# Performance work log

Hardware: AMD Instinct MI355X
Metric: run time of the kernel (lower is better)

Reference implementation:

```python
import jax, jax.numpy as jnp
import numpy as np

B, L, D = 2, 2048, 1024
H, DK, DV = 16, 64, 64
EPS = 1e-6


def setup_inputs() -> dict:
    key = jax.random.key(0)
    ks = jax.random.split(key, 7)
    s = 0.02
    return {
        "x": jax.random.normal(ks[0], (B, L, D), dtype=jnp.float32),
        "Wq": jax.random.normal(ks[1], (D, H * DK), dtype=jnp.float32) * s,
        "Wk": jax.random.normal(ks[2], (D, H * DK), dtype=jnp.float32) * s,
        "Wv": jax.random.normal(ks[3], (D, H * DV), dtype=jnp.float32) * s,
        "Wo": jax.random.normal(ks[4], (H * DV, D), dtype=jnp.float32) * s,
        "ln_gamma": jnp.ones((D,), dtype=jnp.float32),
        "ln_beta": jnp.zeros((D,), dtype=jnp.float32),
    }


def reference(x, Wq, Wk, Wv, Wo, ln_gamma, ln_beta):
    temp = jnp.asarray(DK, x.dtype) ** 0.5
    # projections -> [B, H, L, Dh]
    q = (x @ Wq).reshape(B, L, H, DK).transpose(0, 2, 1, 3)
    k = (x @ Wk).reshape(B, L, H, DK).transpose(0, 2, 1, 3)
    v = (x @ Wv).reshape(B, L, H, DV).transpose(0, 2, 1, 3)
    # naive attention: explicit [B,H,L,L] scores (dropout rate 0 -> identity)
    scores = jnp.einsum("bhqd,bhkd->bhqk", q / temp, k)
    attn = jax.nn.softmax(scores, axis=-1)
    o = jnp.einsum("bhqk,bhkd->bhqd", attn, v)
    o = o.transpose(0, 2, 1, 3).reshape(B, L, H * DV)
    out = o @ Wo + x  # residual
    # LayerNorm(eps=1e-6)
    mu = jnp.mean(out, axis=-1, keepdims=True)
    var = jnp.var(out, axis=-1, keepdims=True)
    return (out - mu) * jax.lax.rsqrt(var + EPS) * ln_gamma + ln_beta
```

## Files before the change

kernel.cpp:

```cpp
#include <hip/hip_runtime.h>


typedef __bf16 bf16;
typedef __bf16 bf16x2 __attribute__((ext_vector_type(2)));
typedef __bf16 bf16x4 __attribute__((ext_vector_type(4)));
typedef __bf16 bf16x8 __attribute__((ext_vector_type(8)));
typedef float floatx4 __attribute__((ext_vector_type(4)));
typedef int intx4 __attribute__((ext_vector_type(4)));

#define MFMA16(a, b, c) __builtin_amdgcn_mfma_f32_16x16x32_bf16((a), (b), (c), 0, 0, 0)

__device__ __forceinline__ void gll16(const bf16* g, bf16* l) {
  __builtin_amdgcn_global_load_lds((const __attribute__((address_space(1))) void*)g,
                                   (__attribute__((address_space(3))) void*)l, 16, 0, 0);
}

__global__ __launch_bounds__(256) void k_prep_x(const float* __restrict__ x, bf16* __restrict__ xb) {
  const int i = (blockIdx.x * 256 + threadIdx.x) * 4;
  const float4 v = *reinterpret_cast<const float4*>(x + i);
  bf16x4 o = {(bf16)v.x, (bf16)v.y, (bf16)v.z, (bf16)v.w};
  *reinterpret_cast<bf16x4*>(xb + i) = o;
}

__global__ __launch_bounds__(256) void k_prep_w(const float* __restrict__ Wq, const float* __restrict__ Wk,
                                                const float* __restrict__ Wv, const float* __restrict__ Wo,
                                                bf16* __restrict__ WT) {
  __shared__ float tile[32][33];
  const int z = blockIdx.z;
  const float* W = (z == 0) ? Wq : (z == 1) ? Wk : (z == 2) ? Wv : Wo;
  const int n0 = blockIdx.x * 32, k0 = blockIdx.y * 32;
  const int tx = threadIdx.x, ty = threadIdx.y;
#pragma unroll
  for (int j = 0; j < 32; j += 8)
    tile[ty + j][tx] = W[(size_t)(k0 + ty + j) * 1024 + n0 + tx];
  __syncthreads();
#pragma unroll
  for (int j = 0; j < 32; j += 8)
    WT[(size_t)(z * 1024 + n0 + ty + j) * 1024 + k0 + tx] = (bf16)tile[tx][ty + j];
}

template <int MODE>
__global__ __launch_bounds__(256) void k_gemm(const bf16* __restrict__ A, const bf16* __restrict__ Bt,
                                              const float* __restrict__ X, float* __restrict__ Y,
                                              bf16* __restrict__ QB, bf16* __restrict__ KB,
                                              bf16* __restrict__ VTB) {
  __shared__ __align__(16) bf16 As[128 * 64];
  __shared__ __align__(16) bf16 Bs[128 * 64];
  const int t = threadIdx.x;
  const int lane = t & 63, wv = t >> 6;
  const int qd = lane >> 4, col = lane & 15;
  const int c7 = col & 7;
  const int wm = wv >> 1, wn = wv & 1;
  const int m0 = blockIdx.x * 128, n0 = blockIdx.y * 128;
  const int srow = wv * 8 + (lane >> 3);
  const int scol = ((lane & 7) ^ (lane >> 3)) * 8;
  const bf16* Ag = A + (size_t)(m0 + srow) * 1024 + scol;
  const bf16* Bg = Bt + (size_t)(n0 + srow) * 1024 + scol;

  floatx4 acc[4][4] = {};

  for (int kt = 0; kt < 1024; kt += 64) {
    __syncthreads();
#pragma unroll
    for (int rd = 0; rd < 4; rd++) {
      gll16(Ag + (size_t)rd * 32 * 1024 + kt, As + (rd * 32 + wv * 8) * 64);
      gll16(Bg + (size_t)rd * 32 * 1024 + kt, Bs + (rd * 32 + wv * 8) * 64);
    }
    __syncthreads();
#pragma unroll
    for (int ks = 0; ks < 2; ks++) {
      bf16x8 af[4], bfr[4];
#pragma unroll
      for (int i = 0; i < 4; i++)
        af[i] = *reinterpret_cast<const bf16x8*>(As + (wm * 64 + i * 16 + col) * 64 + ((ks * 4 + qd) ^ c7) * 8);
#pragma unroll
      for (int i = 0; i < 4; i++)
        bfr[i] = *reinterpret_cast<const bf16x8*>(Bs + (wn * 64 + i * 16 + col) * 64 + ((ks * 4 + qd) ^ c7) * 8);
#pragma unroll
      for (int i = 0; i < 4; i++)
#pragma unroll
        for (int j = 0; j < 4; j++)
          acc[i][j] = MFMA16(af[i], bfr[j], acc[i][j]);
    }
  }

#pragma unroll
  for (int i = 0; i < 4; i++) {
#pragma unroll
    for (int j = 0; j < 4; j++) {
      const int mb = m0 + wm * 64 + i * 16 + qd * 4;
      const int n = n0 + wn * 64 + j * 16 + col;
      if (MODE == 0) {
        const int seg = n >> 10;
        const int h = (n & 1023) >> 6, dd = n & 63;
#pragma unroll
        for (int r = 0; r < 4; r++) {
          const int m = mb + r;
          const int bb = m >> 11, l = m & 2047;
          const float v = acc[i][j][r];
          if (seg == 0)
            QB[((size_t)(bb * 16 + h) * 2048 + l) * 64 + dd] = (bf16)(v * 0.18033688f);
          else if (seg == 1)
            KB[((size_t)(bb * 16 + h) * 2048 + l) * 64 + dd] = (bf16)v;
          else
            VTB[((size_t)(bb * 16 + h) * 64 + dd) * 2048 + l] = (bf16)v;
        }
      } else {
#pragma unroll
        for (int r = 0; r < 4; r++) {
          const int m = mb + r;
          Y[(size_t)m * 1024 + n] = acc[i][j][r] + X[(size_t)m * 1024 + n];
        }
      }
    }
  }
}

__global__ __launch_bounds__(256) void k_attn(const bf16* __restrict__ QB, const bf16* __restrict__ KB,
                                              const bf16* __restrict__ VTB, bf16* __restrict__ OB) {
  __shared__ __align__(16) bf16 Ks0[64 * 64];
  __shared__ __align__(16) bf16 Vs0[64 * 64];
  __shared__ __align__(16) bf16 Ks1[64 * 64];
  __shared__ __align__(16) bf16 Vs1[64 * 64];
  const int t = threadIdx.x;
  const int lane = t & 63, wv = t >> 6;
  const int qd = lane >> 4, col = lane & 15;
  const int c7 = col & 7;
  const int bh = blockIdx.y;
  const int qr = blockIdx.x * 128 + wv * 32;
  const int lrow0 = wv * 8 + (lane >> 3);
  const int swz = ((lane & 7) ^ (lane >> 3)) * 8;
  const int kg0 = ((lrow0 >> 5) << 5) + (((lrow0 >> 2) & 3) << 3) + (((lrow0 >> 4) & 1) << 2) + (lrow0 & 3);
  const int r1 = lrow0 + 32;
  const int kg1 = ((r1 >> 5) << 5) + (((r1 >> 2) & 3) << 3) + (((r1 >> 4) & 1) << 2) + (r1 & 3);
  const bf16* Kg0 = KB + ((size_t)bh * 2048 + kg0) * 64 + swz;
  const bf16* Kg1 = KB + ((size_t)bh * 2048 + kg1) * 64 + swz;
  const bf16* Vg0 = VTB + ((size_t)bh * 64 + lrow0) * 2048 + swz;
  const bf16* Vg1 = VTB + ((size_t)bh * 64 + lrow0 + 32) * 2048 + swz;

  bf16x8 bQ[2][2];
#pragma unroll
  for (int qt = 0; qt < 2; qt++)
#pragma unroll
    for (int s = 0; s < 2; s++)
      bQ[qt][s] = *reinterpret_cast<const bf16x8*>(QB + ((size_t)bh * 2048 + qr + qt * 16 + col) * 64 + s * 32 + qd * 8);

  floatx4 oacc[2][4] = {};
  float lsum[2] = {0.f, 0.f};
  floatx4 scur[2][4];
  int pk[2][4][2];

#define STAGE_TO(KD, VD, i)                               \
  do {                                                    \
    gll16(Kg0 + (size_t)(i) * 4096, KD + (wv * 8) * 64);  \
    gll16(Kg1 + (size_t)(i) * 4096, KD + (32 + wv * 8) * 64); \
    gll16(Vg0 + (i) * 64, VD + (wv * 8) * 64);            \
    gll16(Vg1 + (i) * 64, VD + (32 + wv * 8) * 64);       \
  } while (0)

#define QK_FROM(ks_)                                                                                  \
  do {                                                                                                \
    _Pragma("unroll") for (int nt = 0; nt < 4; nt++) {                                                \
      bf16x8 a0 = *reinterpret_cast<const bf16x8*>(ks_ + (nt * 16 + col) * 64 + (qd ^ c7) * 8);       \
      bf16x8 a1 = *reinterpret_cast<const bf16x8*>(ks_ + (nt * 16 + col) * 64 + ((4 + qd) ^ c7) * 8); \
      _Pragma("unroll") for (int qt = 0; qt < 2; qt++) {                                              \
        floatx4 z = {0.f, 0.f, 0.f, 0.f};                                                             \
        z = MFMA16(a0, bQ[qt][0], z);                                                                 \
        z = MFMA16(a1, bQ[qt][1], z);                                                                 \
        scur[qt][nt] = z;                                                                             \
      }                                                                                               \
    }                                                                                                 \
  } while (0)

#define EXPPACK()                                                                               \
  do {                                                                                          \
    _Pragma("unroll") for (int qt = 0; qt < 2; qt++) {                                          \
      _Pragma("unroll") for (int nt = 0; nt < 4; nt++) {                                        \
        const float e0 = exp2f(scur[qt][nt][0]), e1 = exp2f(scur[qt][nt][1]);                   \
        const float e2 = exp2f(scur[qt][nt][2]), e3 = exp2f(scur[qt][nt][3]);                   \
        lsum[qt] += (e0 + e1) + (e2 + e3);                                                      \
        bf16x2 p01, p23;                                                                        \
        p01[0] = (bf16)e0; p01[1] = (bf16)e1;                                                   \
        p23[0] = (bf16)e2; p23[1] = (bf16)e3;                                                   \
        pk[qt][nt][0] = __builtin_bit_cast(int, p01);                                           \
        pk[qt][nt][1] = __builtin_bit_cast(int, p23);                                           \
      }                                                                                         \
    }                                                                                           \
  } while (0)

#define PV_FROM(vs_)                                                                                  \
  do {                                                                                                \
    bf16x8 bV[4][2];                                                                                  \
    _Pragma("unroll") for (int nd = 0; nd < 4; nd++) {                                                \
      bV[nd][0] = *reinterpret_cast<const bf16x8*>(vs_ + (nd * 16 + col) * 64 + (qd ^ c7) * 8);       \
      bV[nd][1] = *reinterpret_cast<const bf16x8*>(vs_ + (nd * 16 + col) * 64 + ((4 + qd) ^ c7) * 8); \
    }                                                                                                 \
    _Pragma("unroll") for (int qt = 0; qt < 2; qt++) {                                                \
      _Pragma("unroll") for (int s = 0; s < 2; s++) {                                                 \
        intx4 w;                                                                                      \
        w[0] = pk[qt][2 * s][0]; w[1] = pk[qt][2 * s][1];                                             \
        w[2] = pk[qt][2 * s + 1][0]; w[3] = pk[qt][2 * s + 1][1];                                     \
        const bf16x8 aP = __builtin_bit_cast(bf16x8, w);                                              \
        _Pragma("unroll") for (int nd = 0; nd < 4; nd++)                                              \
          oacc[qt][nd] = MFMA16(aP, bV[nd][s], oacc[qt][nd]);                                         \
      }                                                                                               \
    }                                                                                                 \
  } while (0)

  STAGE_TO(Ks0, Vs0, 0);
  __syncthreads();
  for (int ii = 0; ii < 16; ii++) {
    const int i1 = 2 * ii + 1;
    STAGE_TO(Ks1, Vs1, i1);
    QK_FROM(Ks0);
    EXPPACK();
    PV_FROM(Vs0);
    __syncthreads();
    if (i1 < 31) STAGE_TO(Ks0, Vs0, i1 + 1);
    QK_FROM(Ks1);
    EXPPACK();
    PV_FROM(Vs1);
    __syncthreads();
  }

#pragma unroll
  for (int qt = 0; qt < 2; qt++) {
    lsum[qt] += __shfl_xor(lsum[qt], 16);
    lsum[qt] += __shfl_xor(lsum[qt], 32);
  }
  const int bb = bh >> 4, h = bh & 15;
#pragma unroll
  for (int qt = 0; qt < 2; qt++) {
#pragma unroll
    for (int r = 0; r < 4; r++) {
      const float linv = 1.f / __shfl(lsum[qt], qd * 4 + r);
      const size_t m = (size_t)bb * 2048 + qr + qt * 16 + qd * 4 + r;
#pragma unroll
      for (int nd = 0; nd < 4; nd++)
        OB[m * 1024 + h * 64 + nd * 16 + col] = (bf16)(oacc[qt][nd][r] * linv);
    }
  }
#undef STAGE_TO
#undef QK_FROM
#undef EXPPACK
#undef PV_FROM
}

__global__ __launch_bounds__(256) void k_ln(const float* __restrict__ Yin, const float* __restrict__ gamma,
                                            const float* __restrict__ beta, float* __restrict__ out) {
  __shared__ float red[8];
  const int row = blockIdx.x, t = threadIdx.x;
  const float4 v = *reinterpret_cast<const float4*>(Yin + (size_t)row * 1024 + t * 4);
  float s = v.x + v.y + v.z + v.w;
  float ss = v.x * v.x + v.y * v.y + v.z * v.z + v.w * v.w;
#pragma unroll
  for (int d = 1; d < 64; d <<= 1) {
    s += __shfl_xor(s, d);
    ss += __shfl_xor(ss, d);
  }
  if ((t & 63) == 0) {
    red[t >> 6] = s;
    red[4 + (t >> 6)] = ss;
  }
  __syncthreads();
  s = red[0] + red[1] + red[2] + red[3];
  ss = red[4] + red[5] + red[6] + red[7];
  const float mu = s * (1.f / 1024.f);
  const float var = ss * (1.f / 1024.f) - mu * mu;
  const float rs = rsqrtf(var + 1e-6f);
  const float4 g = *reinterpret_cast<const float4*>(gamma + t * 4);
  const float4 bt = *reinterpret_cast<const float4*>(beta + t * 4);
  float4 o;
  o.x = (v.x - mu) * rs * g.x + bt.x;
  o.y = (v.y - mu) * rs * g.y + bt.y;
  o.z = (v.z - mu) * rs * g.z + bt.z;
  o.w = (v.w - mu) * rs * g.w + bt.w;
  *reinterpret_cast<float4*>(out + (size_t)row * 1024 + t * 4) = o;
}

extern "C" void kernel_launch(void* const* d_in, const int* in_sizes, int n_in,
                              void* d_out, int out_size, void* d_ws, size_t ws_size,
                              hipStream_t stream) {
  (void)in_sizes; (void)n_in; (void)out_size; (void)ws_size;
  const float* x = (const float*)d_in[0];
  const float* Wq = (const float*)d_in[1];
  const float* Wk = (const float*)d_in[2];
  const float* Wv = (const float*)d_in[3];
  const float* Wo = (const float*)d_in[4];
  const float* gamma = (const float*)d_in[5];
  const float* beta = (const float*)d_in[6];

  char* ws = (char*)d_ws;
  const size_t MB = 1ull << 20;
  bf16* XB = (bf16*)(ws);
  bf16* OB = (bf16*)(ws);
  bf16* WT = (bf16*)(ws + 8 * MB);
  bf16* QB = (bf16*)(ws + 16 * MB);
  bf16* KB = (bf16*)(ws + 24 * MB);
  bf16* VTB = (bf16*)(ws + 32 * MB);
  float* Y = (float*)(ws + 16 * MB);

  k_prep_x<<<4096, 256, 0, stream>>>(x, XB);
  k_prep_w<<<dim3(32, 32, 4), dim3(32, 8), 0, stream>>>(Wq, Wk, Wv, Wo, WT);
  k_gemm<0><<<dim3(32, 24), 256, 0, stream>>>(XB, WT, nullptr, nullptr, QB, KB, VTB);
  k_attn<<<dim3(16, 32), 256, 0, stream>>>(QB, KB, VTB, OB);
  k_gemm<1><<<dim3(32, 8), 256, 0, stream>>>(OB, WT + (size_t)3072 * 1024, x, Y,
                                             nullptr, nullptr, nullptr);
  k_ln<<<4096, 256, 0, stream>>>(Y, gamma, beta, (float*)d_out);
}
```

Measured before the change: 216.0 us.

## Software-pipeline attention QK ahead of PV, merge prep kernels, bf16 residual buffer

The attention loop is restructured so the QK scores for tile i are computed before the barrier, while the exp/pack and PV of tile i-1 overlap with staging tile i. The PV step is split into two halves that load V fragments on demand, which lowers register pressure. The x-conversion and weight-transpose kernels are merged into one launch. V^T stores are vectorised into 4-element writes. The pre-LayerNorm residual buffer is stored as bf16 instead of fp32 to halve that traffic, at the cost of precision before the normalization.

```diff
diff --git a/kernel.cpp b/kernel.cpp
--- a/kernel.cpp
+++ b/kernel.cpp
@@ -15,21 +15,25 @@
                                    (__attribute__((address_space(3))) void*)l, 16, 0, 0);
 }
 
-__global__ __launch_bounds__(256) void k_prep_x(const float* __restrict__ x, bf16* __restrict__ xb) {
-  const int i = (blockIdx.x * 256 + threadIdx.x) * 4;
-  const float4 v = *reinterpret_cast<const float4*>(x + i);
-  bf16x4 o = {(bf16)v.x, (bf16)v.y, (bf16)v.z, (bf16)v.w};
-  *reinterpret_cast<bf16x4*>(xb + i) = o;
-}
-
-__global__ __launch_bounds__(256) void k_prep_w(const float* __restrict__ Wq, const float* __restrict__ Wk,
-                                                const float* __restrict__ Wv, const float* __restrict__ Wo,
-                                                bf16* __restrict__ WT) {
+__global__ __launch_bounds__(256) void k_prep(const float* __restrict__ x, const float* __restrict__ Wq,
+                                              const float* __restrict__ Wk, const float* __restrict__ Wv,
+                                              const float* __restrict__ Wo, bf16* __restrict__ xb,
+                                              bf16* __restrict__ WT) {
   __shared__ float tile[32][33];
   const int z = blockIdx.z;
+  const int tx = threadIdx.x, ty = threadIdx.y;
+  if (z == 4) {
+    const int base = ((blockIdx.y * 32 + blockIdx.x) * 256 + ty * 32 + tx) * 16;
+#pragma unroll
+    for (int u = 0; u < 4; u++) {
+      const float4 v = *reinterpret_cast<const float4*>(x + base + u * 4);
+      bf16x4 o = {(bf16)v.x, (bf16)v.y, (bf16)v.z, (bf16)v.w};
+      *reinterpret_cast<bf16x4*>(xb + base + u * 4) = o;
+    }
+    return;
+  }
   const float* W = (z == 0) ? Wq : (z == 1) ? Wk : (z == 2) ? Wv : Wo;
   const int n0 = blockIdx.x * 32, k0 = blockIdx.y * 32;
-  const int tx = threadIdx.x, ty = threadIdx.y;
 #pragma unroll
   for (int j = 0; j < 32; j += 8)
     tile[ty + j][tx] = W[(size_t)(k0 + ty + j) * 1024 + n0 + tx];
@@ -41,7 +45,7 @@
 
 template <int MODE>
 __global__ __launch_bounds__(256) void k_gemm(const bf16* __restrict__ A, const bf16* __restrict__ Bt,
-                                              const float* __restrict__ X, float* __restrict__ Y,
+                                              const float* __restrict__ X, bf16* __restrict__ Yb,
                                               bf16* __restrict__ QB, bf16* __restrict__ KB,
                                               bf16* __restrict__ VTB) {
   __shared__ __align__(16) bf16 As[128 * 64];
@@ -93,23 +97,27 @@
       if (MODE == 0) {
         const int seg = n >> 10;
         const int h = (n & 1023) >> 6, dd = n & 63;
+        const int bb = mb >> 11, l0 = mb & 2047;
+        if (seg == 2) {
+          bf16x4 v4;
+#pragma unroll
+          for (int r = 0; r < 4; r++) v4[r] = (bf16)acc[i][j][r];
+          *reinterpret_cast<bf16x4*>(VTB + ((size_t)(bb * 16 + h) * 64 + dd) * 2048 + l0) = v4;
+        } else {
+#pragma unroll
+          for (int r = 0; r < 4; r++) {
+            const float v = acc[i][j][r];
+            if (seg == 0)
+              QB[((size_t)(bb * 16 + h) * 2048 + l0 + r) * 64 + dd] = (bf16)(v * 0.18033688f);
+            else
+              KB[((size_t)(bb * 16 + h) * 2048 + l0 + r) * 64 + dd] = (bf16)v;
+          }
+        }
+      } else {
 #pragma unroll
         for (int r = 0; r < 4; r++) {
           const int m = mb + r;
-          const int bb = m >> 11, l = m & 2047;
-          const float v = acc[i][j][r];
-          if (seg == 0)
-            QB[((size_t)(bb * 16 + h) * 2048 + l) * 64 + dd] = (bf16)(v * 0.18033688f);
-          else if (seg == 1)
-            KB[((size_t)(bb * 16 + h) * 2048 + l) * 64 + dd] = (bf16)v;
-          else
-            VTB[((size_t)(bb * 16 + h) * 64 + dd) * 2048 + l] = (bf16)v;
-        }
-      } else {
-#pragma unroll
-        for (int r = 0; r < 4; r++) {
-          const int m = mb + r;
-          Y[(size_t)m * 1024 + n] = acc[i][j][r] + X[(size_t)m * 1024 + n];
+          Yb[(size_t)m * 1024 + n] = (bf16)(acc[i][j][r] + X[(size_t)m * 1024 + n]);
         }
       }
     }
@@ -118,10 +126,8 @@
 
 __global__ __launch_bounds__(256) void k_attn(const bf16* __restrict__ QB, const bf16* __restrict__ KB,
                                               const bf16* __restrict__ VTB, bf16* __restrict__ OB) {
-  __shared__ __align__(16) bf16 Ks0[64 * 64];
-  __shared__ __align__(16) bf16 Vs0[64 * 64];
-  __shared__ __align__(16) bf16 Ks1[64 * 64];
-  __shared__ __align__(16) bf16 Vs1[64 * 64];
+  __shared__ __align__(16) bf16 Ks[2][64 * 64];
+  __shared__ __align__(16) bf16 Vs[2][64 * 64];
   const int t = threadIdx.x;
   const int lane = t & 63, wv = t >> 6;
   const int qd = lane >> 4, col = lane & 15;
@@ -150,16 +156,18 @@
   floatx4 scur[2][4];
   int pk[2][4][2];
 
-#define STAGE_TO(KD, VD, i)                               \
-  do {                                                    \
-    gll16(Kg0 + (size_t)(i) * 4096, KD + (wv * 8) * 64);  \
-    gll16(Kg1 + (size_t)(i) * 4096, KD + (32 + wv * 8) * 64); \
-    gll16(Vg0 + (i) * 64, VD + (wv * 8) * 64);            \
-    gll16(Vg1 + (i) * 64, VD + (32 + wv * 8) * 64);       \
+#define STAGE(i)                                                  \
+  do {                                                            \
+    const int b_ = (i) & 1;                                       \
+    gll16(Kg0 + (size_t)(i) * 4096, &Ks[b_][(wv * 8) * 64]);      \
+    gll16(Kg1 + (size_t)(i) * 4096, &Ks[b_][(32 + wv * 8) * 64]); \
+    gll16(Vg0 + (i) * 64, &Vs[b_][(wv * 8) * 64]);                \
+    gll16(Vg1 + (i) * 64, &Vs[b_][(32 + wv * 8) * 64]);           \
   } while (0)
 
-#define QK_FROM(ks_)                                                                                  \
+#define QK(i)                                                                                         \
   do {                                                                                                \
+    const bf16* ks_ = Ks[(i) & 1];                                                                    \
     _Pragma("unroll") for (int nt = 0; nt < 4; nt++) {                                                \
       bf16x8 a0 = *reinterpret_cast<const bf16x8*>(ks_ + (nt * 16 + col) * 64 + (qd ^ c7) * 8);       \
       bf16x8 a1 = *reinterpret_cast<const bf16x8*>(ks_ + (nt * 16 + col) * 64 + ((4 + qd) ^ c7) * 8); \
@@ -172,10 +180,11 @@
     }                                                                                                 \
   } while (0)
 
-#define EXPPACK()                                                                               \
+#define EXPPACK_S(sl)                                                                           \
   do {                                                                                          \
     _Pragma("unroll") for (int qt = 0; qt < 2; qt++) {                                          \
-      _Pragma("unroll") for (int nt = 0; nt < 4; nt++) {                                        \
+      _Pragma("unroll") for (int nn = 0; nn < 2; nn++) {                                        \
+        const int nt = 2 * (sl) + nn;                                                           \
         const float e0 = exp2f(scur[qt][nt][0]), e1 = exp2f(scur[qt][nt][1]);                   \
         const float e2 = exp2f(scur[qt][nt][2]), e3 = exp2f(scur[qt][nt][3]);                   \
         lsum[qt] += (e0 + e1) + (e2 + e3);                                                      \
@@ -188,40 +197,39 @@
     }                                                                                           \
   } while (0)
 
-#define PV_FROM(vs_)                                                                                  \
+#define PV_S(i, sl)                                                                                   \
   do {                                                                                                \
-    bf16x8 bV[4][2];                                                                                  \
-    _Pragma("unroll") for (int nd = 0; nd < 4; nd++) {                                                \
-      bV[nd][0] = *reinterpret_cast<const bf16x8*>(vs_ + (nd * 16 + col) * 64 + (qd ^ c7) * 8);       \
-      bV[nd][1] = *reinterpret_cast<const bf16x8*>(vs_ + (nd * 16 + col) * 64 + ((4 + qd) ^ c7) * 8); \
-    }                                                                                                 \
+    const bf16* vs_ = Vs[(i) & 1];                                                                    \
     _Pragma("unroll") for (int qt = 0; qt < 2; qt++) {                                                \
-      _Pragma("unroll") for (int s = 0; s < 2; s++) {                                                 \
-        intx4 w;                                                                                      \
-        w[0] = pk[qt][2 * s][0]; w[1] = pk[qt][2 * s][1];                                             \
-        w[2] = pk[qt][2 * s + 1][0]; w[3] = pk[qt][2 * s + 1][1];                                     \
-        const bf16x8 aP = __builtin_bit_cast(bf16x8, w);                                              \
-        _Pragma("unroll") for (int nd = 0; nd < 4; nd++)                                              \
-          oacc[qt][nd] = MFMA16(aP, bV[nd][s], oacc[qt][nd]);                                         \
+      intx4 w;                                                                                        \
+      w[0] = pk[qt][2 * (sl)][0]; w[1] = pk[qt][2 * (sl)][1];                                         \
+      w[2] = pk[qt][2 * (sl) + 1][0]; w[3] = pk[qt][2 * (sl) + 1][1];                                 \
+      const bf16x8 aP = __builtin_bit_cast(bf16x8, w);                                                \
+      _Pragma("unroll") for (int nd = 0; nd < 4; nd++) {                                              \
+        const bf16x8 bV = *reinterpret_cast<const bf16x8*>(                                           \
+            vs_ + (nd * 16 + col) * 64 + (((sl)*4 + qd) ^ c7) * 8);                                   \
+        oacc[qt][nd] = MFMA16(aP, bV, oacc[qt][nd]);                                                  \
       }                                                                                               \
     }                                                                                                 \
   } while (0)
 
-  STAGE_TO(Ks0, Vs0, 0);
+  STAGE(0);
   __syncthreads();
-  for (int ii = 0; ii < 16; ii++) {
-    const int i1 = 2 * ii + 1;
-    STAGE_TO(Ks1, Vs1, i1);
-    QK_FROM(Ks0);
-    EXPPACK();
-    PV_FROM(Vs0);
+  QK(0);
+  for (int i = 1; i < 32; i++) {
     __syncthreads();
-    if (i1 < 31) STAGE_TO(Ks0, Vs0, i1 + 1);
-    QK_FROM(Ks1);
-    EXPPACK();
-    PV_FROM(Vs1);
+    STAGE(i);
+    EXPPACK_S(0);
+    PV_S(i - 1, 0);
+    EXPPACK_S(1);
+    PV_S(i - 1, 1);
     __syncthreads();
-  }
+    QK(i);
+  }
+  EXPPACK_S(0);
+  PV_S(31, 0);
+  EXPPACK_S(1);
+  PV_S(31, 1);
 
 #pragma unroll
   for (int qt = 0; qt < 2; qt++) {
@@ -240,19 +248,20 @@
         OB[m * 1024 + h * 64 + nd * 16 + col] = (bf16)(oacc[qt][nd][r] * linv);
     }
   }
-#undef STAGE_TO
-#undef QK_FROM
-#undef EXPPACK
-#undef PV_FROM
-}
-
-__global__ __launch_bounds__(256) void k_ln(const float* __restrict__ Yin, const float* __restrict__ gamma,
+#undef STAGE
+#undef QK
+#undef EXPPACK_S
+#undef PV_S
+}
+
+__global__ __launch_bounds__(256) void k_ln(const bf16* __restrict__ Yb, const float* __restrict__ gamma,
                                             const float* __restrict__ beta, float* __restrict__ out) {
   __shared__ float red[8];
   const int row = blockIdx.x, t = threadIdx.x;
-  const float4 v = *reinterpret_cast<const float4*>(Yin + (size_t)row * 1024 + t * 4);
-  float s = v.x + v.y + v.z + v.w;
-  float ss = v.x * v.x + v.y * v.y + v.z * v.z + v.w * v.w;
+  const bf16x4 vb = *reinterpret_cast<const bf16x4*>(Yb + (size_t)row * 1024 + t * 4);
+  const float v0 = (float)vb[0], v1 = (float)vb[1], v2 = (float)vb[2], v3 = (float)vb[3];
+  float s = v0 + v1 + v2 + v3;
+  float ss = v0 * v0 + v1 * v1 + v2 * v2 + v3 * v3;
 #pragma unroll
   for (int d = 1; d < 64; d <<= 1) {
     s += __shfl_xor(s, d);
@@ -271,10 +280,10 @@
   const float4 g = *reinterpret_cast<const float4*>(gamma + t * 4);
   const float4 bt = *reinterpret_cast<const float4*>(beta + t * 4);
   float4 o;
-  o.x = (v.x - mu) * rs * g.x + bt.x;
-  o.y = (v.y - mu) * rs * g.y + bt.y;
-  o.z = (v.z - mu) * rs * g.z + bt.z;
-  o.w = (v.w - mu) * rs * g.w + bt.w;
+  o.x = (v0 - mu) * rs * g.x + bt.x;
+  o.y = (v1 - mu) * rs * g.y + bt.y;
+  o.z = (v2 - mu) * rs * g.z + bt.z;
+  o.w = (v3 - mu) * rs * g.w + bt.w;
   *reinterpret_cast<float4*>(out + (size_t)row * 1024 + t * 4) = o;
 }
 
@@ -298,13 +307,12 @@
   bf16* QB = (bf16*)(ws + 16 * MB);
   bf16* KB = (bf16*)(ws + 24 * MB);
   bf16* VTB = (bf16*)(ws + 32 * MB);
-  float* Y = (float*)(ws + 16 * MB);
-
-  k_prep_x<<<4096, 256, 0, stream>>>(x, XB);
-  k_prep_w<<<dim3(32, 32, 4), dim3(32, 8), 0, stream>>>(Wq, Wk, Wv, Wo, WT);
+  bf16* Yb = (bf16*)(ws + 16 * MB);
+
+  k_prep<<<dim3(32, 32, 5), dim3(32, 8), 0, stream>>>(x, Wq, Wk, Wv, Wo, XB, WT);
   k_gemm<0><<<dim3(32, 24), 256, 0, stream>>>(XB, WT, nullptr, nullptr, QB, KB, VTB);
   k_attn<<<dim3(16, 32), 256, 0, stream>>>(QB, KB, VTB, OB);
-  k_gemm<1><<<dim3(32, 8), 256, 0, stream>>>(OB, WT + (size_t)3072 * 1024, x, Y,
+  k_gemm<1><<<dim3(32, 8), 256, 0, stream>>>(OB, WT + (size_t)3072 * 1024, x, Yb,
                                              nullptr, nullptr, nullptr);
-  k_ln<<<4096, 256, 0, stream>>>(Y, gamma, beta, (float*)d_out);
-}
+  k_ln<<<4096, 256, 0, stream>>>(Yb, gamma, beta, (float*)d_out);
+}
```

After: 212.4 us. No clear change (-1.7%).
